# Performance work log

Hardware: AMD Instinct MI355X
Metric: run time of the kernel (lower is better)

The kernel has to match this reference:

```python
import jax, jax.numpy as jnp
import numpy as np

THRESHOLD = 1.5
MIN_AREA = 3
B, H, W = 8, 1024, 1024


def _label_components(mask):
    """8-connectivity connected-component labeling by min-index propagation.
    mask: [B,H,W] bool. Returns int32 labels [B,H,W]; each component is labeled
    by the minimum global flat index of its pixels; background pixels = B*H*W.
    Labels are globally unique across the batch (matches sort_labels' per-batch
    unique relabeling up to a label permutation).
    """
    N = B * H * W
    SENT = jnp.int32(N)
    flat = jnp.arange(N, dtype=jnp.int32).reshape(B, H, W)
    lab0 = jnp.where(mask, flat, SENT)

    def neighbor_min(lab):
        p = jnp.pad(lab, ((0, 0), (1, 1), (1, 1)), constant_values=N)
        m = lab
        for dr in (-1, 0, 1):
            for dc in (-1, 0, 1):
                if dr == 0 and dc == 0:
                    continue
                m = jnp.minimum(m, p[:, 1 + dr:1 + dr + H, 1 + dc:1 + dc + W])
        return jnp.where(mask, m, SENT)

    def cond(state):
        return state[1]

    def body(state):
        lab, _ = state
        new = neighbor_min(lab)
        return new, jnp.any(new != lab)

    lab, _ = jax.lax.while_loop(cond, body, (lab0, jnp.array(True)))
    return lab


def setup_inputs() -> dict:
    key = jax.random.key(0)
    x = jax.random.normal(key, (B, H, W // 1), dtype=jnp.float32)
    return {"input_tensor": x.reshape(B, 1, H, W)}


def reference(input_tensor):
    """Dense encoding of the original ragged output: for every pixel belonging
    to a cluster with area > MIN_AREA, emit the cluster's max value and the
    (row, col) of the first (lowest flat index) occurrence of that max;
    background / small-cluster pixels get (0, -1, -1). Since THRESHOLD > 0,
    max over masked_fill(0) in the original equals max over cluster pixels.
    """
    x = input_tensor[:, 0]                  # [B,H,W]
    N = B * H * W
    nseg = N + 1                            # last segment = background
    mask = (x >= THRESHOLD)
    ids = _label_components(mask).reshape(-1)          # [N] int32 in [0, N]
    vals = x.reshape(-1)
    fg = mask.reshape(-1)

    area = jax.ops.segment_sum(fg.astype(jnp.float32), ids, num_segments=nseg)
    cmax = jax.ops.segment_max(vals, ids, num_segments=nseg)

    within = jnp.tile(jnp.arange(H * W, dtype=jnp.int32), B)  # flat idx in image
    is_max = (vals == cmax[ids]) & fg
    cand = jnp.where(is_max, within, jnp.int32(H * W))
    amin = jax.ops.segment_min(cand, ids, num_segments=nseg)  # first argmax

    valid = fg & (area[ids] > MIN_AREA)
    out_max = jnp.where(valid, cmax[ids], jnp.float32(0.0)).reshape(B, H, W)
    aidx = amin[ids]
    row = jnp.where(valid, aidx // W, jnp.int32(-1)).reshape(B, H, W)
    col = jnp.where(valid, aidx % W, jnp.int32(-1)).reshape(B, H, W)
    return out_max, row, col
```

## Files before the change

### kernel.cpp

```cpp
#include <hip/hip_runtime.h>
#include <stdint.h>

#define THRESH 1.5f
constexpr int NPIX = 8 * 1024 * 1024;
constexpr int HW   = 1024 * 1024;
constexpr int WW   = 1024;
constexpr int NWORD = NPIX / 32;
constexpr int WPR   = WW / 32;

constexpr int BLK     = 256;
constexpr int GRD_PX4 = NPIX / (BLK * 4);
constexpr int GRD_W   = NWORD / BLK;

constexpr int SPB        = 640;
constexpr int BASE_SLOTS = GRD_W * SPB;
constexpr int OVF_SLOTS  = 16384;
constexpr int CAP        = BASE_SLOTS + OVF_SLOTS;

constexpr int WLSTRIDE = 1024;

__device__ __forceinline__ int find_root(const int* __restrict__ P, int x) {
    int p = P[x];
    while (p != x && p < NPIX) { x = p; p = P[x]; }
    return x;
}

__device__ __forceinline__ void merge(int* P, int a, int b) {
    int ra = find_root(P, a);
    int rb = find_root(P, b);
    while (ra != rb) {
        if (ra < rb) { int t = ra; ra = rb; rb = t; }
        int old = atomicCAS(&P[ra], ra, rb);
        if (old == ra) break;
        ra = find_root(P, old);
        rb = find_root(P, rb);
    }
}

__global__ void mask_init_k(const float* __restrict__ x, int* __restrict__ parent,
                            unsigned* __restrict__ mask, uint2* __restrict__ wl,
                            int* __restrict__ wl_cnt, int* __restrict__ ovf) {
    __shared__ unsigned s_nib[BLK];
    __shared__ int s_rank;
    int t  = threadIdx.x;
    int gt = blockIdx.x * BLK + t;
    int i4 = gt * 4;
    float4 v = *(const float4*)(x + i4);
    unsigned nib = (unsigned)(v.x >= THRESH) | ((unsigned)(v.y >= THRESH) << 1) |
                   ((unsigned)(v.z >= THRESH) << 2) | ((unsigned)(v.w >= THRESH) << 3);
    *(int4*)(parent + i4) = make_int4(i4, i4 + 1, i4 + 2, i4 + 3);
    if (t == 0) s_rank = 0;
    s_nib[t] = nib;
    __syncthreads();
    if ((t & 7) == 0) {
        unsigned w = 0;
        #pragma unroll
        for (int k = 0; k < 8; k++) w |= s_nib[t + k] << (4 * k);
        mask[gt >> 3] = w;
    }
    int nfg = __popc(nib);
    if (nfg) {
        int r = atomicAdd(&s_rank, nfg);
        uint2* dst = wl + (size_t)blockIdx.x * WLSTRIDE;
        if (nib & 1u) dst[r++] = make_uint2((unsigned)i4,     __float_as_uint(v.x));
        if (nib & 2u) dst[r++] = make_uint2((unsigned)i4 + 1, __float_as_uint(v.y));
        if (nib & 4u) dst[r++] = make_uint2((unsigned)i4 + 2, __float_as_uint(v.z));
        if (nib & 8u) dst[r++] = make_uint2((unsigned)i4 + 3, __float_as_uint(v.w));
    }
    __syncthreads();
    if (t == 0) wl_cnt[blockIdx.x] = s_rank;
    if (gt == 0) *ovf = 0;
}

__global__ void union_k(const unsigned* __restrict__ mask, int* __restrict__ parent) {
    int w = blockIdx.x * BLK + threadIdx.x;
    unsigned cur = mask[w];
    if (!cur) return;
    int r  = (w >> 5) & (WW - 1);
    int cw = w & (WPR - 1);
    unsigned prev = (cw > 0) ? mask[w - 1] : 0u;
    unsigned above = 0u, abovePrev = 0u, aboveNext = 0u;
    if (r > 0) {
        above     = mask[w - WPR];
        abovePrev = (cw > 0)       ? mask[w - WPR - 1] : 0u;
        aboveNext = (cw < WPR - 1) ? mask[w - WPR + 1] : 0u;
    }
    int base = w << 5;
    unsigned mW  = cur & ((cur   << 1) | (prev      >> 31));
    unsigned mN  = cur & above;
    unsigned mNW = cur & ((above << 1) | (abovePrev >> 31));
    unsigned mNE = cur & ((above >> 1) | ((aboveNext & 1u) << 31));
    while (mW)  { int b = __ffs(mW)  - 1; mW  &= mW  - 1; merge(parent, base + b, base + b - 1); }
    while (mN)  { int b = __ffs(mN)  - 1; mN  &= mN  - 1; merge(parent, base + b, base + b - WW); }
    while (mNW) { int b = __ffs(mNW) - 1; mNW &= mNW - 1; merge(parent, base + b, base + b - WW - 1); }
    while (mNE) { int b = __ffs(mNE) - 1; mNE &= mNE - 1; merge(parent, base + b, base + b - WW + 1); }
}

__global__ void claim_k(const unsigned* __restrict__ mask, int* __restrict__ parent,
                        int* __restrict__ cnt, unsigned long long* __restrict__ best,
                        int* __restrict__ ovf) {
    __shared__ int s_cnt;
    if (threadIdx.x == 0) s_cnt = 0;
    __syncthreads();
    int w = blockIdx.x * BLK + threadIdx.x;
    unsigned cur = mask[w];
    int base = w << 5;
    while (cur) {
        int b = __ffs(cur) - 1; cur &= cur - 1;
        int p = base + b;
        int root = find_root(parent, p);
        if (root == p) {
            int rank = atomicAdd(&s_cnt, 1);
            int slot;
            if (rank < SPB) slot = blockIdx.x * SPB + rank;
            else { int o = atomicAdd(ovf, 1); slot = BASE_SLOTS + (o < OVF_SLOTS ? o : OVF_SLOTS - 1); }
            cnt[slot] = 0; best[slot] = 0ull;
            parent[p] = NPIX + slot;
        } else {
            parent[p] = root;
        }
    }
}

__device__ __forceinline__ int compact_id(const int* __restrict__ P, int p) {
    int e = P[p];
    if (e < NPIX) e = P[e];
    return e - NPIX;
}

__global__ void stats_k(const uint2* __restrict__ wl, const int* __restrict__ wl_cnt,
                        const int* __restrict__ parent, int* __restrict__ cnt,
                        unsigned long long* __restrict__ best) {
    int region = blockIdx.x;
    int c = wl_cnt[region];
    const uint2* src = wl + (size_t)region * WLSTRIDE;
    for (int j = threadIdx.x; j < c; j += 64) {
        uint2 e = src[j];
        int p = (int)e.x;
        int cid = compact_id(parent, p);
        if (cid < 0 || cid >= CAP) continue;
        atomicAdd(&cnt[cid], 1);
        unsigned within = (unsigned)(p & (HW - 1));
        unsigned long long pk =
            ((unsigned long long)e.y << 32) | (unsigned long long)(~within);
        atomicMax(&best[cid], pk);
    }
}

__device__ __forceinline__ void lookup_one(const int* __restrict__ parent,
                                           const int* __restrict__ cnt,
                                           const unsigned long long* __restrict__ best,
                                           int p, float& om, float& orow, float& ocol) {
    int cid = compact_id(parent, p);
    if (cid >= 0 && cid < CAP && cnt[cid] > 3) {
        unsigned long long pk = best[cid];
        om   = __uint_as_float((unsigned)(pk >> 32));
        unsigned idx = ~((unsigned)pk);
        orow = (float)(idx >> 10);
        ocol = (float)(idx & (WW - 1));
    }
}

__global__ void out_k(const unsigned* __restrict__ mask, const int* __restrict__ parent,
                      const int* __restrict__ cnt,
                      const unsigned long long* __restrict__ best,
                      float* __restrict__ o) {
    int t = blockIdx.x * BLK + threadIdx.x;
    unsigned nib = (mask[t >> 3] >> ((t & 7) * 4)) & 0xFu;
    int i4 = t * 4;
    float4 m  = make_float4(0.f, 0.f, 0.f, 0.f);
    float4 rr = make_float4(-1.f, -1.f, -1.f, -1.f);
    float4 cc = make_float4(-1.f, -1.f, -1.f, -1.f);
    if (nib) {
        if (nib & 1u) lookup_one(parent, cnt, best, i4,     m.x, rr.x, cc.x);
        if (nib & 2u) lookup_one(parent, cnt, best, i4 + 1, m.y, rr.y, cc.y);
        if (nib & 4u) lookup_one(parent, cnt, best, i4 + 2, m.z, rr.z, cc.z);
        if (nib & 8u) lookup_one(parent, cnt, best, i4 + 3, m.w, rr.w, cc.w);
    }
    *(float4*)(o + i4)            = m;
    *(float4*)(o + NPIX + i4)     = rr;
    *(float4*)(o + 2 * NPIX + i4) = cc;
}

extern "C" void kernel_launch(void* const* d_in, const int* in_sizes, int n_in,
                              void* d_out, int out_size, void* d_ws, size_t ws_size,
                              hipStream_t stream) {
    const float* x = (const float*)d_in[0];
    float* o = (float*)d_out;

    char* base = (char*)d_ws;
    int* parent = (int*)base;
    size_t off = (size_t)NPIX * 4;
    unsigned long long* best = (unsigned long long*)(base + off);  off += (size_t)CAP * 8;
    int* cnt       = (int*)(base + off);                           off += (size_t)CAP * 4;
    unsigned* mask = (unsigned*)(base + off);                      off += (size_t)NWORD * 4;
    int* wl_cnt    = (int*)(base + off);                           off += (size_t)GRD_PX4 * 4;
    uint2* wl      = (uint2*)(base + off);                         off += (size_t)GRD_PX4 * WLSTRIDE * 8;
    int* ovf       = (int*)(base + off);

    mask_init_k<<<GRD_PX4, BLK, 0, stream>>>(x, parent, mask, wl, wl_cnt, ovf);
    union_k    <<<GRD_W,   BLK, 0, stream>>>(mask, parent);
    claim_k    <<<GRD_W,   BLK, 0, stream>>>(mask, parent, cnt, best, ovf);
    stats_k    <<<GRD_PX4, 64,  0, stream>>>(wl, wl_cnt, parent, cnt, best);
    out_k      <<<GRD_PX4, BLK, 0, stream>>>(mask, parent, cnt, best, o);
}
```

Measured before the change: 202.9 us.

## Fuse output defaults into mask init and scatter results from foreground worklist

```diff
diff --git a/kernel.cpp b/kernel.cpp
--- a/kernel.cpp
+++ b/kernel.cpp
@@ -39,7 +39,8 @@
 
 __global__ void mask_init_k(const float* __restrict__ x, int* __restrict__ parent,
                             unsigned* __restrict__ mask, uint2* __restrict__ wl,
-                            int* __restrict__ wl_cnt, int* __restrict__ ovf) {
+                            int* __restrict__ wl_cnt, int* __restrict__ ovf,
+                            float* __restrict__ o) {
     __shared__ unsigned s_nib[BLK];
     __shared__ int s_rank;
     int t  = threadIdx.x;
@@ -48,7 +49,11 @@
     float4 v = *(const float4*)(x + i4);
     unsigned nib = (unsigned)(v.x >= THRESH) | ((unsigned)(v.y >= THRESH) << 1) |
                    ((unsigned)(v.z >= THRESH) << 2) | ((unsigned)(v.w >= THRESH) << 3);
-    *(int4*)(parent + i4) = make_int4(i4, i4 + 1, i4 + 2, i4 + 3);
+    *(float4*)(o + i4)            = make_float4(0.f, 0.f, 0.f, 0.f);
+    *(float4*)(o + NPIX + i4)     = make_float4(-1.f, -1.f, -1.f, -1.f);
+    *(float4*)(o + 2 * NPIX + i4) = make_float4(-1.f, -1.f, -1.f, -1.f);
+    if (nib)
+        *(int4*)(parent + i4) = make_int4(i4, i4 + 1, i4 + 2, i4 + 3);
     if (t == 0) s_rank = 0;
     s_nib[t] = nib;
     __syncthreads();
@@ -128,17 +133,18 @@
     return e - NPIX;
 }
 
-__global__ void stats_k(const uint2* __restrict__ wl, const int* __restrict__ wl_cnt,
+__global__ void stats_k(uint2* __restrict__ wl, const int* __restrict__ wl_cnt,
                         const int* __restrict__ parent, int* __restrict__ cnt,
                         unsigned long long* __restrict__ best) {
     int region = blockIdx.x;
     int c = wl_cnt[region];
-    const uint2* src = wl + (size_t)region * WLSTRIDE;
+    uint2* src = wl + (size_t)region * WLSTRIDE;
     for (int j = threadIdx.x; j < c; j += 64) {
         uint2 e = src[j];
         int p = (int)e.x;
         int cid = compact_id(parent, p);
-        if (cid < 0 || cid >= CAP) continue;
+        if (cid < 0 || cid >= CAP) { src[j].y = 0xFFFFFFFFu; continue; }
+        src[j].y = (unsigned)cid;
         atomicAdd(&cnt[cid], 1);
         unsigned within = (unsigned)(p & (HW - 1));
         unsigned long long pk =
@@ -147,39 +153,26 @@
     }
 }
 
-__device__ __forceinline__ void lookup_one(const int* __restrict__ parent,
-                                           const int* __restrict__ cnt,
-                                           const unsigned long long* __restrict__ best,
-                                           int p, float& om, float& orow, float& ocol) {
-    int cid = compact_id(parent, p);
-    if (cid >= 0 && cid < CAP && cnt[cid] > 3) {
-        unsigned long long pk = best[cid];
-        om   = __uint_as_float((unsigned)(pk >> 32));
-        unsigned idx = ~((unsigned)pk);
-        orow = (float)(idx >> 10);
-        ocol = (float)(idx & (WW - 1));
+__global__ void scatter_k(const uint2* __restrict__ wl, const int* __restrict__ wl_cnt,
+                          const int* __restrict__ cnt,
+                          const unsigned long long* __restrict__ best,
+                          float* __restrict__ o) {
+    int region = blockIdx.x;
+    int c = wl_cnt[region];
+    const uint2* src = wl + (size_t)region * WLSTRIDE;
+    for (int j = threadIdx.x; j < c; j += 64) {
+        uint2 e = src[j];
+        unsigned cid = e.y;
+        if (cid >= (unsigned)CAP) continue;
+        if (cnt[cid] > 3) {
+            unsigned long long pk = best[cid];
+            unsigned idx = ~((unsigned)pk);
+            int p = (int)e.x;
+            o[p]            = __uint_as_float((unsigned)(pk >> 32));
+            o[p + NPIX]     = (float)(idx >> 10);
+            o[p + 2 * NPIX] = (float)(idx & (WW - 1));
+        }
     }
-}
-
-__global__ void out_k(const unsigned* __restrict__ mask, const int* __restrict__ parent,
-                      const int* __restrict__ cnt,
-                      const unsigned long long* __restrict__ best,
-                      float* __restrict__ o) {
-    int t = blockIdx.x * BLK + threadIdx.x;
-    unsigned nib = (mask[t >> 3] >> ((t & 7) * 4)) & 0xFu;
-    int i4 = t * 4;
-    float4 m  = make_float4(0.f, 0.f, 0.f, 0.f);
-    float4 rr = make_float4(-1.f, -1.f, -1.f, -1.f);
-    float4 cc = make_float4(-1.f, -1.f, -1.f, -1.f);
-    if (nib) {
-        if (nib & 1u) lookup_one(parent, cnt, best, i4,     m.x, rr.x, cc.x);
-        if (nib & 2u) lookup_one(parent, cnt, best, i4 + 1, m.y, rr.y, cc.y);
-        if (nib & 4u) lookup_one(parent, cnt, best, i4 + 2, m.z, rr.z, cc.z);
-        if (nib & 8u) lookup_one(parent, cnt, best, i4 + 3, m.w, rr.w, cc.w);
-    }
-    *(float4*)(o + i4)            = m;
-    *(float4*)(o + NPIX + i4)     = rr;
-    *(float4*)(o + 2 * NPIX + i4) = cc;
 }
 
 extern "C" void kernel_launch(void* const* d_in, const int* in_sizes, int n_in,
@@ -198,9 +191,9 @@
     uint2* wl      = (uint2*)(base + off);                         off += (size_t)GRD_PX4 * WLSTRIDE * 8;
     int* ovf       = (int*)(base + off);
 
-    mask_init_k<<<GRD_PX4, BLK, 0, stream>>>(x, parent, mask, wl, wl_cnt, ovf);
+    mask_init_k<<<GRD_PX4, BLK, 0, stream>>>(x, parent, mask, wl, wl_cnt, ovf, o);
     union_k    <<<GRD_W,   BLK, 0, stream>>>(mask, parent);
     claim_k    <<<GRD_W,   BLK, 0, stream>>>(mask, parent, cnt, best, ovf);
     stats_k    <<<GRD_PX4, 64,  0, stream>>>(wl, wl_cnt, parent, cnt, best);
-    out_k      <<<GRD_PX4, BLK, 0, stream>>>(mask, parent, cnt, best, o);
+    scatter_k  <<<GRD_PX4, 64,  0, stream>>>(wl, wl_cnt, cnt, best, o);
 }
```

After: 206.9 us. No clear change (+2.0%).
